# Kernel optimization log

Measured on AMD Instinct MI355X. Metric: run time of the kernel, lower is better.

The kernel has to match this reference:

```python
import jax, jax.numpy as jnp
import numpy as np

N, E, DIM, HID, TEMB = 50000, 600000, 128, 128, 8
IN_DIM = 3 * DIM + TEMB  # zi, zj, |zi-zj|, type_emb


def setup_inputs() -> dict:
    key = jax.random.key(0)
    ks = jax.random.split(key, 16)
    s = lambda *sh: 1.0 / np.sqrt(sh[-1])
    return {
        "z": jax.random.normal(ks[0], (N, DIM), jnp.float32),
        "edge_index": jax.random.randint(ks[1], (2, E), 0, N, jnp.int64),
        "edge_type": jax.random.randint(ks[2], (E,), 0, 2, jnp.int64),
        "type_emb": jax.random.normal(ks[3], (2, TEMB), jnp.float32),
        "ew1": jax.random.normal(ks[4], (HID, IN_DIM), jnp.float32) * s(HID, IN_DIM),
        "eb1": jnp.zeros((HID,), jnp.float32),
        "ew2": jax.random.normal(ks[5], (1, HID), jnp.float32) * s(1, HID),
        "eb2": jnp.zeros((1,), jnp.float32),
        "mw1": jax.random.normal(ks[6], (DIM, DIM), jnp.float32) * s(DIM, DIM),
        "mb1": jnp.zeros((DIM,), jnp.float32),
        "mw2": jax.random.normal(ks[7], (DIM, DIM), jnp.float32) * s(DIM, DIM),
        "mb2": jnp.zeros((DIM,), jnp.float32),
        "gamma": jnp.ones((DIM,), jnp.float32),
        "beta": jnp.zeros((DIM,), jnp.float32),
    }


def reference(z, edge_index, edge_type, type_emb, ew1, eb1, ew2, eb2,
              mw1, mb1, mw2, mb2, gamma, beta):
    src, dst = edge_index[0], edge_index[1]
    zi = z[src]          # [E, DIM]
    zj = z[dst]          # [E, DIM]
    te = type_emb[edge_type]  # [E, TEMB]
    e_in = jnp.concatenate([zi, zj, jnp.abs(zi - zj), te], axis=1)  # [E, IN_DIM]

    # edge MLP -> scalar weight per edge, sigmoid squashed
    h = jax.nn.relu(e_in @ ew1.T + eb1)
    w = jax.nn.sigmoid((h @ ew2.T + eb2)[:, 0])  # [E]

    n = z.shape[0]
    # numerically-stable segment softmax over edges grouped by src
    max_per_src = jnp.full((n,), -1e9, dtype=z.dtype).at[src].max(w)
    w_exp = jnp.exp(w - max_per_src[src])
    sum_per_src = jax.ops.segment_sum(w_exp, src, num_segments=n)
    alpha = w_exp / (sum_per_src[src] + 1e-12)  # [E]

    # message MLP on destination features, weighted by alpha
    msg = (jax.nn.relu(zj @ mw1.T + mb1) @ mw2.T + mb2) * alpha[:, None]  # [E, DIM]
    agg = jax.ops.segment_sum(msg, src, num_segments=n)  # [N, DIM]

    # residual + LayerNorm (dropout is identity in eval mode)
    x = z + agg
    mu = jnp.mean(x, axis=-1, keepdims=True)
    var = jnp.mean(jnp.square(x - mu), axis=-1, keepdims=True)
    out = (x - mu) * jax.lax.rsqrt(var + 1e-5) * gamma + beta
    return (out, alpha)
```

## Files before the change

### kernel.cpp

```cpp
#include <hip/hip_runtime.h>
#include <math.h>

constexpr int NN  = 50000;
constexpr int NE  = 600000;
constexpr int D   = 128;
constexpr int IND = 392;

constexpr int NB_NODE = (NN + 127) / 128;
constexpr int NB_FILL = (NE + 511) / 512;

typedef __attribute__((ext_vector_type(8))) short bf16x8;
typedef __attribute__((ext_vector_type(4))) float f32x4;

__device__ __forceinline__ float4 ld4(const float* p) { return *reinterpret_cast<const float4*>(p); }

__device__ __forceinline__ unsigned short f2bf(float f) {
  unsigned int u = __float_as_uint(f);
  u += 0x7fffu + ((u >> 16) & 1u);
  return (unsigned short)(u >> 16);
}
__device__ __forceinline__ float bf2f(unsigned short s) {
  return __uint_as_float(((unsigned int)s) << 16);
}

__global__ __launch_bounds__(256) void k_preph(
    const float* __restrict__ ew1, const float* __restrict__ type_emb,
    const float* __restrict__ mw1, const float* __restrict__ mw2,
    const int* __restrict__ ei,
    unsigned short* __restrict__ Wab, unsigned short* __restrict__ Wbb,
    unsigned short* __restrict__ Wcb,
    unsigned short* __restrict__ m1b, unsigned short* __restrict__ m2b,
    float* __restrict__ tvg, int* __restrict__ deg)
{
  const int b = blockIdx.x, t = threadIdx.x;
  if (b < 64) {
    int g = b * 256 + t;
    int o = g >> 7, k = g & 127;
    Wab[g] = f2bf(ew1[o * IND + k]);
    Wbb[g] = f2bf(ew1[o * IND + 128 + k]);
    Wcb[g] = f2bf(ew1[o * IND + 256 + k]);
    m1b[g] = f2bf(mw1[g]);
    m2b[g] = f2bf(mw2[g]);
    if (b == 0) {
      int oo = t & 127, ty = t >> 7;
      float s = 0.f;
#pragma unroll
      for (int j = 0; j < 8; ++j) s += ew1[oo * IND + 384 + j] * type_emb[ty * 8 + j];
      tvg[ty * 128 + oo] = s;
    }
  } else {
    int e = (b - 64) * 256 + t;
    if (e < NE) atomicAdd(&deg[ei[e]], 1);
  }
}

__device__ __forceinline__ void mm1(
    const unsigned short (*X)[136], const unsigned short (*W)[136],
    int me, int r, int q, f32x4 acc[8])
{
#pragma unroll
  for (int ks = 0; ks < 4; ++ks) {
    bf16x8 a = *reinterpret_cast<const bf16x8*>(&X[me + r][ks * 32 + q * 8]);
#pragma unroll
    for (int nt = 0; nt < 8; ++nt) {
      bf16x8 b = *reinterpret_cast<const bf16x8*>(&W[nt * 16 + r][ks * 32 + q * 8]);
      acc[nt] = __builtin_amdgcn_mfma_f32_16x16x32_bf16(a, b, acc[nt], 0, 0, 0);
    }
  }
}

__global__ __launch_bounds__(512, 2) void k_nodefill(
    const float* __restrict__ z,
    const unsigned short* __restrict__ Wab, const unsigned short* __restrict__ Wbb,
    const unsigned short* __restrict__ m1b, const unsigned short* __restrict__ m2b,
    const float* __restrict__ mb1, const float* __restrict__ mb2,
    unsigned short* __restrict__ Ab, unsigned short* __restrict__ Bb,
    unsigned short* __restrict__ Mb, unsigned short* __restrict__ zb,
    const int* __restrict__ ei, int* __restrict__ cursor,
    int* __restrict__ eid, int* __restrict__ de_perm, int* __restrict__ inv)
{
  __shared__ unsigned short Xh[128][136];
  __shared__ unsigned short Wh[128][136];
  const int t = threadIdx.x;

  if (blockIdx.x >= NB_NODE) {
    int e = (blockIdx.x - NB_NODE) * 512 + t;
    if (e < NE) {
      int pos = atomicAdd(&cursor[ei[e]], 1);
      eid[pos] = e;
      de_perm[pos] = ei[NE + e];
      inv[e] = pos;
    }
    return;
  }

  const int n0 = blockIdx.x * 128;

#pragma unroll
  for (int it = 0; it < 8; ++it) {
    int f = it * 512 + t, rr = f >> 5, c4 = (f & 31) * 4;
    int n = n0 + rr; if (n >= NN) n = NN - 1;
    float4 v = ld4(&z[(size_t)n * D + c4]);
    ushort4 hi;
    hi.x = f2bf(v.x); hi.y = f2bf(v.y); hi.z = f2bf(v.z); hi.w = f2bf(v.w);
    *reinterpret_cast<ushort4*>(&Xh[rr][c4]) = hi;
    if (n0 + rr < NN)
      *reinterpret_cast<ushort4*>(&zb[(size_t)(n0 + rr) * D + c4]) = hi;
  }
#pragma unroll
  for (int it = 0; it < 4; ++it) {
    int f = it * 512 + t, row = f >> 4, c8 = (f & 15) * 8;
    *reinterpret_cast<bf16x8*>(&Wh[row][c8]) =
        *reinterpret_cast<const bf16x8*>(&Wab[row * 128 + c8]);
  }
  __syncthreads();

  const int l = t & 63, q = l >> 4, r = l & 15;
  const int me = (t >> 6) * 16;

  f32x4 acc[8];

#pragma unroll
  for (int nt = 0; nt < 8; ++nt) acc[nt] = (f32x4){0.f, 0.f, 0.f, 0.f};
  mm1(Xh, Wh, me, r, q, acc);
#pragma unroll
  for (int nt = 0; nt < 8; ++nt)
#pragma unroll
    for (int i = 0; i < 4; ++i) {
      int n = n0 + me + q * 4 + i;
      if (n < NN) Ab[(size_t)n * D + nt * 16 + r] = f2bf(acc[nt][i]);
    }
  __syncthreads();

#pragma unroll
  for (int it = 0; it < 4; ++it) {
    int f = it * 512 + t, row = f >> 4, c8 = (f & 15) * 8;
    *reinterpret_cast<bf16x8*>(&Wh[row][c8]) =
        *reinterpret_cast<const bf16x8*>(&Wbb[row * 128 + c8]);
  }
  __syncthreads();
#pragma unroll
  for (int nt = 0; nt < 8; ++nt) acc[nt] = (f32x4){0.f, 0.f, 0.f, 0.f};
  mm1(Xh, Wh, me, r, q, acc);
#pragma unroll
  for (int nt = 0; nt < 8; ++nt)
#pragma unroll
    for (int i = 0; i < 4; ++i) {
      int n = n0 + me + q * 4 + i;
      if (n < NN) Bb[(size_t)n * D + nt * 16 + r] = f2bf(acc[nt][i]);
    }
  __syncthreads();

#pragma unroll
  for (int it = 0; it < 4; ++it) {
    int f = it * 512 + t, row = f >> 4, c8 = (f & 15) * 8;
    *reinterpret_cast<bf16x8*>(&Wh[row][c8]) =
        *reinterpret_cast<const bf16x8*>(&m1b[row * 128 + c8]);
  }
  __syncthreads();
#pragma unroll
  for (int nt = 0; nt < 8; ++nt) acc[nt] = (f32x4){0.f, 0.f, 0.f, 0.f};
  mm1(Xh, Wh, me, r, q, acc);
#pragma unroll
  for (int nt = 0; nt < 8; ++nt) {
    int col = nt * 16 + r;
    float b1 = mb1[col];
#pragma unroll
    for (int i = 0; i < 4; ++i)
      Xh[me + q * 4 + i][col] = f2bf(fmaxf(acc[nt][i] + b1, 0.0f));
  }
  __syncthreads();

#pragma unroll
  for (int it = 0; it < 4; ++it) {
    int f = it * 512 + t, row = f >> 4, c8 = (f & 15) * 8;
    *reinterpret_cast<bf16x8*>(&Wh[row][c8]) =
        *reinterpret_cast<const bf16x8*>(&m2b[row * 128 + c8]);
  }
  __syncthreads();
#pragma unroll
  for (int nt = 0; nt < 8; ++nt) acc[nt] = (f32x4){0.f, 0.f, 0.f, 0.f};
  mm1(Xh, Wh, me, r, q, acc);
#pragma unroll
  for (int nt = 0; nt < 8; ++nt) {
    int col = nt * 16 + r;
    float b2 = mb2[col];
#pragma unroll
    for (int i = 0; i < 4; ++i) {
      int n = n0 + me + q * 4 + i;
      if (n < NN) Mb[(size_t)n * D + col] = f2bf(acc[nt][i] + b2);
    }
  }
}

constexpr int SNB = 196;

__global__ __launch_bounds__(256) void k_scan1(const int* __restrict__ deg,
                                               int* __restrict__ pre,
                                               int* __restrict__ bsum)
{
  __shared__ int ps[256];
  const int t = threadIdx.x, b = blockIdx.x;
  const int i = b * 256 + t;
  int v = (i < NN) ? deg[i] : 0;
  ps[t] = v;
  __syncthreads();
  for (int off = 1; off < 256; off <<= 1) {
    int u = (t >= off) ? ps[t - off] : 0;
    __syncthreads();
    ps[t] += u;
    __syncthreads();
  }
  pre[i] = ps[t] - v;
  if (t == 255) bsum[b] = ps[255];
}

__global__ __launch_bounds__(256) void k_scan23(const int* __restrict__ pre,
                                                const int* __restrict__ bsum,
                                                int* __restrict__ rowptr,
                                                int* __restrict__ cursor)
{
  __shared__ int ps[256];
  const int t = threadIdx.x, b = blockIdx.x;
  int v = (t < SNB) ? bsum[t] : 0;
  ps[t] = v;
  __syncthreads();
  for (int off = 1; off < 256; off <<= 1) {
    int u = (t >= off) ? ps[t - off] : 0;
    __syncthreads();
    ps[t] += u;
    __syncthreads();
  }
  const int base = (b == 0) ? 0 : ps[b - 1];
  const int i = b * 256 + t;
  if (i < NN) {
    int vv = pre[i] + base;
    rowptr[i] = vv;
    cursor[i] = vv;
  }
  if (i == 0) rowptr[NN] = NE;
}

__global__ __launch_bounds__(512, 6) void k_edge_mfma(
    const unsigned short* __restrict__ zb, const int* __restrict__ ei,
    const int* __restrict__ etype,
    const unsigned short* __restrict__ Wcb, const float* __restrict__ tvg,
    const float* __restrict__ eb1, const float* __restrict__ ew2,
    const float* __restrict__ eb2,
    const unsigned short* __restrict__ Ab, const unsigned short* __restrict__ Bb,
    const int* __restrict__ eid, const int* __restrict__ de_perm,
    float* __restrict__ wexp_perm)
{
  __shared__ unsigned short Xb[128 * 128];
  __shared__ unsigned short Wb[64 * 128];
  __shared__ unsigned short se[128], de[128];
  __shared__ unsigned char  tyg[128];

  const int t = threadIdx.x;
  const int nx = gridDim.x >> 3;
  const int sb = (blockIdx.x & 7) * nx + (blockIdx.x >> 3);
  const int e0 = sb * 128;

  if (t < 128) {
    int pos = e0 + t;
    if (pos < NE) {
      int e  = eid[pos];
      se[t]  = (unsigned short)ei[e];
      de[t]  = (unsigned short)de_perm[pos];
      tyg[t] = (unsigned char)etype[e];
    } else { se[t] = 0; de[t] = 0; tyg[t] = 0; }
  }
#pragma unroll
  for (int it = 0; it < 2; ++it) {
    int f = it * 512 + t, row = f >> 4, c = f & 15;
    int a = (row * 256 + c * 16) ^ ((row & 7) << 4);
    *reinterpret_cast<bf16x8*>((char*)Wb + a) =
        *reinterpret_cast<const bf16x8*>(&Wcb[row * 128 + c * 8]);
  }
  __syncthreads();

#pragma unroll
  for (int it = 0; it < 8; ++it) {
    int f = it * 512 + t, r = f >> 5, c4 = f & 31;
    ushort4 a4 = *reinterpret_cast<const ushort4*>(&zb[(size_t)se[r] * D + c4 * 4]);
    ushort4 b4 = *reinterpret_cast<const ushort4*>(&zb[(size_t)de[r] * D + c4 * 4]);
    ushort4 v;
    v.x = f2bf(fabsf(bf2f(a4.x) - bf2f(b4.x)));
    v.y = f2bf(fabsf(bf2f(a4.y) - bf2f(b4.y)));
    v.z = f2bf(fabsf(bf2f(a4.z) - bf2f(b4.z)));
    v.w = f2bf(fabsf(bf2f(a4.w) - bf2f(b4.w)));
    int a = (r * 256 + c4 * 8) ^ ((r & 7) << 4);
    *reinterpret_cast<ushort4*>((char*)Xb + a) = v;
  }
  __syncthreads();

  const int l = t & 63, q = l >> 4, r = l & 15;
  const int me = (t >> 6) * 16;

  f32x4 acc[8];
#pragma unroll
  for (int nt = 0; nt < 8; ++nt) acc[nt] = (f32x4){0.f, 0.f, 0.f, 0.f};

#pragma unroll
  for (int ks = 0; ks < 4; ++ks) {
    int xa = ((me + r) * 256 + ks * 64 + q * 16) ^ ((r & 7) << 4);
    bf16x8 a = *reinterpret_cast<const bf16x8*>((const char*)Xb + xa);
#pragma unroll
    for (int ntl = 0; ntl < 4; ++ntl) {
      int wrow = ntl * 16 + r;
      int wa = (wrow * 256 + ks * 64 + q * 16) ^ ((wrow & 7) << 4);
      bf16x8 b = *reinterpret_cast<const bf16x8*>((const char*)Wb + wa);
      acc[ntl] = __builtin_amdgcn_mfma_f32_16x16x32_bf16(a, b, acc[ntl], 0, 0, 0);
    }
  }
  __syncthreads();

#pragma unroll
  for (int it = 0; it < 2; ++it) {
    int f = it * 512 + t, row = f >> 4, c = f & 15;
    int a = (row * 256 + c * 16) ^ ((row & 7) << 4);
    *reinterpret_cast<bf16x8*>((char*)Wb + a) =
        *reinterpret_cast<const bf16x8*>(&Wcb[(64 + row) * 128 + c * 8]);
  }
  __syncthreads();

#pragma unroll
  for (int ks = 0; ks < 4; ++ks) {
    int xa = ((me + r) * 256 + ks * 64 + q * 16) ^ ((r & 7) << 4);
    bf16x8 a = *reinterpret_cast<const bf16x8*>((const char*)Xb + xa);
#pragma unroll
    for (int ntl = 0; ntl < 4; ++ntl) {
      int wrow = ntl * 16 + r;
      int wa = (wrow * 256 + ks * 64 + q * 16) ^ ((wrow & 7) << 4);
      bf16x8 b = *reinterpret_cast<const bf16x8*>((const char*)Wb + wa);
      acc[4 + ntl] = __builtin_amdgcn_mfma_f32_16x16x32_bf16(a, b, acc[4 + ntl], 0, 0, 0);
    }
  }

  int s[4], dd[4], ty[4];
#pragma unroll
  for (int i = 0; i < 4; ++i) {
    int el = me + q * 4 + i;
    s[i] = se[el]; dd[i] = de[el]; ty[i] = tyg[el];
  }
  float p[4] = {0.f, 0.f, 0.f, 0.f};
#pragma unroll
  for (int nt = 0; nt < 8; ++nt) {
    int col = nt * 16 + r;
    float e1  = eb1[col], w2 = ew2[col];
    float tva = tvg[col], tvb = tvg[128 + col];
#pragma unroll
    for (int i = 0; i < 4; ++i) {
      float h = acc[nt][i] + bf2f(Ab[(size_t)s[i] * D + col])
              + bf2f(Bb[(size_t)dd[i] * D + col]) + (ty[i] ? tvb : tva) + e1;
      p[i] += fmaxf(h, 0.f) * w2;
    }
  }
#pragma unroll
  for (int m = 1; m < 16; m <<= 1) {
#pragma unroll
    for (int i = 0; i < 4; ++i) p[i] += __shfl_xor(p[i], m);
  }
  if (r == 0) {
    float b2 = eb2[0];
#pragma unroll
    for (int i = 0; i < 4; ++i) {
      int pos = e0 + me + q * 4 + i;
      if (pos < NE) {
        float w = 1.0f / (1.0f + expf(-(p[i] + b2)));
        wexp_perm[pos] = expf(w);
      }
    }
  }
}

__global__ __launch_bounds__(256) void k_agg(
    const float* __restrict__ z, const float* __restrict__ wexp_perm,
    const unsigned short* __restrict__ Mb, const int* __restrict__ rowptr,
    const int* __restrict__ de_perm,
    const float* __restrict__ gamma, const float* __restrict__ beta,
    float* __restrict__ out, float* __restrict__ sumw)
{
  const int t = threadIdx.x;
  const int n = blockIdx.x * 4 + (t >> 6);
  const int l = t & 63;
  const int start = rowptr[n], end = rowptr[n + 1];

  float tot = 0.f;
  for (int base = start; base < end; base += 64) {
    if (base + l < end) tot += wexp_perm[base + l];
  }
#pragma unroll
  for (int off = 32; off; off >>= 1) tot += __shfl_xor(tot, off);
  if (l == 0) sumw[n] = tot;
  const float inv = 1.0f / (tot + 1e-12f);

  float2 acc = make_float2(0.f, 0.f);
  for (int base = start; base < end; base += 64) {
    int cnt = min(64, end - base);
    int dd = 0;
    float al = 0.f;
    if (l < cnt) {
      int pos = base + l;
      al = wexp_perm[pos] * inv;
      dd = de_perm[pos];
    }
    int i = 0;
    for (; i + 8 <= cnt; i += 8) {
      float a[8]; int d[8]; ushort2 m[8];
#pragma unroll
      for (int j = 0; j < 8; ++j) {
        a[j] = __shfl(al, i + j);
        d[j] = __shfl(dd, i + j);
      }
#pragma unroll
      for (int j = 0; j < 8; ++j)
        m[j] = *reinterpret_cast<const ushort2*>(&Mb[(size_t)d[j] * D + l * 2]);
#pragma unroll
      for (int j = 0; j < 8; ++j) {
        acc.x = fmaf(a[j], bf2f(m[j].x), acc.x);
        acc.y = fmaf(a[j], bf2f(m[j].y), acc.y);
      }
    }
    for (; i < cnt; ++i) {
      float a = __shfl(al, i);
      int   d = __shfl(dd, i);
      ushort2 m = *reinterpret_cast<const ushort2*>(&Mb[(size_t)d * D + l * 2]);
      acc.x = fmaf(a, bf2f(m.x), acc.x);
      acc.y = fmaf(a, bf2f(m.y), acc.y);
    }
  }

  float2 xz = *reinterpret_cast<const float2*>(&z[(size_t)n * D + l * 2]);
  float x0 = xz.x + acc.x, x1 = xz.y + acc.y;
  float s = x0 + x1;
#pragma unroll
  for (int off = 32; off; off >>= 1) s += __shfl_xor(s, off);
  const float mu = s * (1.0f / 128.0f);
  float d0 = x0 - mu, d1 = x1 - mu;
  float q = d0 * d0 + d1 * d1;
#pragma unroll
  for (int off = 32; off; off >>= 1) q += __shfl_xor(q, off);
  const float rstd = rsqrtf(q * (1.0f / 128.0f) + 1e-5f);
  float2 g = *reinterpret_cast<const float2*>(&gamma[l * 2]);
  float2 b = *reinterpret_cast<const float2*>(&beta[l * 2]);
  float2 o = make_float2(d0 * rstd * g.x + b.x, d1 * rstd * g.y + b.y);
  *reinterpret_cast<float2*>(&out[(size_t)n * D + l * 2]) = o;
}

__global__ __launch_bounds__(256) void k_alpha(
    const int* __restrict__ ei, const int* __restrict__ inv,
    const float* __restrict__ wexp_perm, const float* __restrict__ sumw,
    float* __restrict__ alpha_out)
{
  int e = blockIdx.x * 256 + threadIdx.x;
  if (e < NE) {
    float we = wexp_perm[inv[e]];
    float sm = sumw[ei[e]];
    alpha_out[e] = we / (sm + 1e-12f);
  }
}

extern "C" void kernel_launch(void* const* d_in, const int* in_sizes, int n_in,
                              void* d_out, int out_size, void* d_ws, size_t ws_size,
                              hipStream_t stream)
{
  const float* z        = (const float*)d_in[0];
  const int*   ei       = (const int*)d_in[1];
  const int*   etype    = (const int*)d_in[2];
  const float* type_emb = (const float*)d_in[3];
  const float* ew1      = (const float*)d_in[4];
  const float* eb1      = (const float*)d_in[5];
  const float* ew2      = (const float*)d_in[6];
  const float* eb2      = (const float*)d_in[7];
  const float* mw1      = (const float*)d_in[8];
  const float* mb1      = (const float*)d_in[9];
  const float* mw2      = (const float*)d_in[10];
  const float* mb2      = (const float*)d_in[11];
  const float* gamma    = (const float*)d_in[12];
  const float* beta     = (const float*)d_in[13];

  float*          ws        = (float*)d_ws;
  unsigned short* Ab        = (unsigned short*)(ws);
  unsigned short* Bb        = (unsigned short*)(ws + 3200000);
  unsigned short* Mb        = (unsigned short*)(ws + 6400000);
  unsigned short* zb        = (unsigned short*)(ws + 9600000);
  float*          wexp_perm = ws + 12800000;
  int*            deg       = (int*)(ws + 13400000);
  int*            rowptr    = deg + 50000;
  int*            cursor    = rowptr + 50004;
  int*            eid       = cursor + 50000;
  int*            de_perm   = eid + 600000;
  unsigned short* Wcb       = (unsigned short*)(ws + 14800000);
  float*          tvg       = ws + 14810000;
  unsigned short* Wab       = (unsigned short*)(ws + 14820000);
  unsigned short* Wbb       = (unsigned short*)(ws + 14830000);
  unsigned short* m1b       = (unsigned short*)(ws + 14840000);
  unsigned short* m2b       = (unsigned short*)(ws + 14850000);
  int*            pre       = (int*)(ws + 14880000);
  int*            bsum      = (int*)(ws + 14940000);
  int*            inv       = (int*)(ws + 15000000);
  float*          sumw      = ws + 15700000;

  float* out       = (float*)d_out;
  float* alpha_out = out + (size_t)NN * D;

  hipMemsetAsync(deg, 0, 50000 * sizeof(int), stream);

  k_preph<<<64 + (NE + 255) / 256, 256, 0, stream>>>(
      ew1, type_emb, mw1, mw2, ei,
      Wab, Wbb, Wcb, m1b, m2b, tvg, deg);
  k_scan1<<<SNB, 256, 0, stream>>>(deg, pre, bsum);
  k_scan23<<<SNB, 256, 0, stream>>>(pre, bsum, rowptr, cursor);
  k_nodefill<<<NB_NODE + NB_FILL, 512, 0, stream>>>(
      z, Wab, Wbb, m1b, m2b, mb1, mb2, Ab, Bb, Mb, zb,
      ei, cursor, eid, de_perm, inv);
  k_edge_mfma<<<(NE + 127) / 128, 512, 0, stream>>>(zb, ei, etype, Wcb, tvg,
                                                    eb1, ew2, eb2, Ab, Bb,
                                                    eid, de_perm, wexp_perm);
  k_agg<<<NN / 4, 256, 0, stream>>>(z, wexp_perm, Mb, rowptr, de_perm,
                                    gamma, beta, out, sumw);
  k_alpha<<<(NE + 255) / 256, 256, 0, stream>>>(ei, inv, wexp_perm, sumw,
                                                alpha_out);
}
```

Before: 218.3 us.

## Fuse alpha output into aggregation kernel and read edge weights directly from global

Removes the separate alpha kernel, along with the inv permutation array and the per-node sum buffer. The aggregation kernel now writes alpha straight to its original edge position through eid, at the cost of scattered stores. The edge MFMA kernel drops its shared-memory staging of the weight matrix and the barriers around it, loading B fragments directly from global or cache. Its launch bound rises to 8 blocks for higher occupancy, with a risk of register pressure or spills.

```diff
diff --git a/kernel.cpp b/kernel.cpp
--- a/kernel.cpp
+++ b/kernel.cpp
@@ -77,7 +77,7 @@
     unsigned short* __restrict__ Ab, unsigned short* __restrict__ Bb,
     unsigned short* __restrict__ Mb, unsigned short* __restrict__ zb,
     const int* __restrict__ ei, int* __restrict__ cursor,
-    int* __restrict__ eid, int* __restrict__ de_perm, int* __restrict__ inv)
+    int* __restrict__ eid, int* __restrict__ de_perm)
 {
   __shared__ unsigned short Xh[128][136];
   __shared__ unsigned short Wh[128][136];
@@ -89,7 +89,6 @@
       int pos = atomicAdd(&cursor[ei[e]], 1);
       eid[pos] = e;
       de_perm[pos] = ei[NE + e];
-      inv[e] = pos;
     }
     return;
   }
@@ -241,7 +240,7 @@
   if (i == 0) rowptr[NN] = NE;
 }
 
-__global__ __launch_bounds__(512, 6) void k_edge_mfma(
+__global__ __launch_bounds__(512, 8) void k_edge_mfma(
     const unsigned short* __restrict__ zb, const int* __restrict__ ei,
     const int* __restrict__ etype,
     const unsigned short* __restrict__ Wcb, const float* __restrict__ tvg,
@@ -252,7 +251,6 @@
     float* __restrict__ wexp_perm)
 {
   __shared__ unsigned short Xb[128 * 128];
-  __shared__ unsigned short Wb[64 * 128];
   __shared__ unsigned short se[128], de[128];
   __shared__ unsigned char  tyg[128];
 
@@ -269,13 +267,6 @@
       de[t]  = (unsigned short)de_perm[pos];
       tyg[t] = (unsigned char)etype[e];
     } else { se[t] = 0; de[t] = 0; tyg[t] = 0; }
-  }
-#pragma unroll
-  for (int it = 0; it < 2; ++it) {
-    int f = it * 512 + t, row = f >> 4, c = f & 15;
-    int a = (row * 256 + c * 16) ^ ((row & 7) << 4);
-    *reinterpret_cast<bf16x8*>((char*)Wb + a) =
-        *reinterpret_cast<const bf16x8*>(&Wcb[row * 128 + c * 8]);
   }
   __syncthreads();
 
@@ -306,34 +297,10 @@
     int xa = ((me + r) * 256 + ks * 64 + q * 16) ^ ((r & 7) << 4);
     bf16x8 a = *reinterpret_cast<const bf16x8*>((const char*)Xb + xa);
 #pragma unroll
-    for (int ntl = 0; ntl < 4; ++ntl) {
-      int wrow = ntl * 16 + r;
-      int wa = (wrow * 256 + ks * 64 + q * 16) ^ ((wrow & 7) << 4);
-      bf16x8 b = *reinterpret_cast<const bf16x8*>((const char*)Wb + wa);
-      acc[ntl] = __builtin_amdgcn_mfma_f32_16x16x32_bf16(a, b, acc[ntl], 0, 0, 0);
-    }
-  }
-  __syncthreads();
-
-#pragma unroll
-  for (int it = 0; it < 2; ++it) {
-    int f = it * 512 + t, row = f >> 4, c = f & 15;
-    int a = (row * 256 + c * 16) ^ ((row & 7) << 4);
-    *reinterpret_cast<bf16x8*>((char*)Wb + a) =
-        *reinterpret_cast<const bf16x8*>(&Wcb[(64 + row) * 128 + c * 8]);
-  }
-  __syncthreads();
-
-#pragma unroll
-  for (int ks = 0; ks < 4; ++ks) {
-    int xa = ((me + r) * 256 + ks * 64 + q * 16) ^ ((r & 7) << 4);
-    bf16x8 a = *reinterpret_cast<const bf16x8*>((const char*)Xb + xa);
-#pragma unroll
-    for (int ntl = 0; ntl < 4; ++ntl) {
-      int wrow = ntl * 16 + r;
-      int wa = (wrow * 256 + ks * 64 + q * 16) ^ ((wrow & 7) << 4);
-      bf16x8 b = *reinterpret_cast<const bf16x8*>((const char*)Wb + wa);
-      acc[4 + ntl] = __builtin_amdgcn_mfma_f32_16x16x32_bf16(a, b, acc[4 + ntl], 0, 0, 0);
+    for (int nt = 0; nt < 8; ++nt) {
+      bf16x8 b = *reinterpret_cast<const bf16x8*>(
+          &Wcb[(nt * 16 + r) * 128 + ks * 32 + q * 8]);
+      acc[nt] = __builtin_amdgcn_mfma_f32_16x16x32_bf16(a, b, acc[nt], 0, 0, 0);
     }
   }
 
@@ -377,9 +344,9 @@
 __global__ __launch_bounds__(256) void k_agg(
     const float* __restrict__ z, const float* __restrict__ wexp_perm,
     const unsigned short* __restrict__ Mb, const int* __restrict__ rowptr,
-    const int* __restrict__ de_perm,
+    const int* __restrict__ eid, const int* __restrict__ de_perm,
     const float* __restrict__ gamma, const float* __restrict__ beta,
-    float* __restrict__ out, float* __restrict__ sumw)
+    float* __restrict__ out, float* __restrict__ alpha_out)
 {
   const int t = threadIdx.x;
   const int n = blockIdx.x * 4 + (t >> 6);
@@ -392,7 +359,6 @@
   }
 #pragma unroll
   for (int off = 32; off; off >>= 1) tot += __shfl_xor(tot, off);
-  if (l == 0) sumw[n] = tot;
   const float inv = 1.0f / (tot + 1e-12f);
 
   float2 acc = make_float2(0.f, 0.f);
@@ -404,6 +370,7 @@
       int pos = base + l;
       al = wexp_perm[pos] * inv;
       dd = de_perm[pos];
+      alpha_out[eid[pos]] = al;
     }
     int i = 0;
     for (; i + 8 <= cnt; i += 8) {
@@ -446,19 +413,6 @@
   float2 b = *reinterpret_cast<const float2*>(&beta[l * 2]);
   float2 o = make_float2(d0 * rstd * g.x + b.x, d1 * rstd * g.y + b.y);
   *reinterpret_cast<float2*>(&out[(size_t)n * D + l * 2]) = o;
-}
-
-__global__ __launch_bounds__(256) void k_alpha(
-    const int* __restrict__ ei, const int* __restrict__ inv,
-    const float* __restrict__ wexp_perm, const float* __restrict__ sumw,
-    float* __restrict__ alpha_out)
-{
-  int e = blockIdx.x * 256 + threadIdx.x;
-  if (e < NE) {
-    float we = wexp_perm[inv[e]];
-    float sm = sumw[ei[e]];
-    alpha_out[e] = we / (sm + 1e-12f);
-  }
 }
 
 extern "C" void kernel_launch(void* const* d_in, const int* in_sizes, int n_in,
@@ -499,8 +453,6 @@
   unsigned short* m2b       = (unsigned short*)(ws + 14850000);
   int*            pre       = (int*)(ws + 14880000);
   int*            bsum      = (int*)(ws + 14940000);
-  int*            inv       = (int*)(ws + 15000000);
-  float*          sumw      = ws + 15700000;
 
   float* out       = (float*)d_out;
   float* alpha_out = out + (size_t)NN * D;
@@ -514,12 +466,10 @@
   k_scan23<<<SNB, 256, 0, stream>>>(pre, bsum, rowptr, cursor);
   k_nodefill<<<NB_NODE + NB_FILL, 512, 0, stream>>>(
       z, Wab, Wbb, m1b, m2b, mb1, mb2, Ab, Bb, Mb, zb,
-      ei, cursor, eid, de_perm, inv);
+      ei, cursor, eid, de_perm);
   k_edge_mfma<<<(NE + 127) / 128, 512, 0, stream>>>(zb, ei, etype, Wcb, tvg,
                                                     eb1, ew2, eb2, Ab, Bb,
                                                     eid, de_perm, wexp_perm);
-  k_agg<<<NN / 4, 256, 0, stream>>>(z, wexp_perm, Mb, rowptr, de_perm,
-                                    gamma, beta, out, sumw);
-  k_alpha<<<(NE + 255) / 256, 256, 0, stream>>>(ei, inv, wexp_perm, sumw,
-                                                alpha_out);
-}
+  k_agg<<<NN / 4, 256, 0, stream>>>(z, wexp_perm, Mb, rowptr, eid, de_perm,
+                                    gamma, beta, out, alpha_out);
+}
```

New measurement: 357.1 us. 63.6% more time.
